# Kernel optimization log

Measured on AMD Instinct MI355X. Metric: run time of the kernel, lower is better.

The kernel has to match this reference:

```python
import jax, jax.numpy as jnp
import numpy as np

N_RET = 8192
N_LGN = 2048
SQUARE_SIZE = 10.0
NEIGHBOURHOOD = 1.0
MU_WTS = 2.5
SIGMA_WTS = 0.14
ETA = 0.1


def setup_inputs() -> dict:
    key = jax.random.key(0)
    ks = jax.random.split(key, 6)
    # retina topology on a [0, square_size]^2 plane
    topo = jax.random.uniform(ks[0], (N_RET, 2), dtype=jnp.float32) * SQUARE_SIZE
    # pairwise distances [N_ret, N_ret]
    d = jnp.sqrt(jnp.sum((topo[:, None, :] - topo[None, :, :]) ** 2, axis=-1))
    # per-node neighbourhood weights: normal(mu, sigma) masked to dist <= neighbourhood_size
    w = MU_WTS + SIGMA_WTS * jax.random.normal(ks[1], (N_RET, N_RET), dtype=jnp.float32)
    retina_weights = jnp.where(d <= NEIGHBOURHOOD, w, 0.0)
    # per-node firing threshold (Node internals: threshold ~ N(70, 2), same family as LGN)
    retina_threshold = 70.0 + 2.0 * jax.random.normal(ks[2], (N_RET,), dtype=jnp.float32)
    # LGN weights, row-normalised to mean mu_wts as in __init__
    lw = MU_WTS + SIGMA_WTS * jax.random.normal(ks[3], (N_LGN, N_RET), dtype=jnp.float32)
    lgn_weights = lw / jnp.mean(lw, axis=1, keepdims=True) * MU_WTS
    lgn_threshold = 70.0 + 2.0 * jax.random.normal(ks[4], (N_LGN,), dtype=jnp.float32)
    is_firing = (jax.random.uniform(ks[5], (N_RET,)) < 0.2).astype(jnp.float32)
    return {
        "retina_weights": retina_weights,
        "retina_threshold": retina_threshold,
        "lgn_weights": lgn_weights,
        "lgn_threshold": lgn_threshold,
        "is_firing": is_firing,
    }


def reference(retina_weights, retina_threshold, lgn_weights, lgn_threshold, is_firing):
    # Per-node sparse neighbourhood matvec (the Python loop over nodes, vectorised):
    node_x = retina_weights @ is_firing                       # [N_ret]
    new_firing = (node_x > retina_threshold).astype(retina_weights.dtype)
    # LGN activation + relu (lgn_act[lgn_act < 0] = 0)
    lgn_act = jnp.maximum(lgn_weights @ new_firing, 0.0)      # [N_lgn]
    act = jnp.maximum(lgn_act - lgn_threshold, 0.0)
    # winner-take-all update of the argmax LGN row
    idx = jnp.argmax(act)
    val = act[idx]
    row = lgn_weights[idx]
    # original does two additions of 0.5 * eta * val * active_neurons
    row = row + 0.5 * (ETA * val * new_firing)
    row = row + 0.5 * (ETA * val * new_firing)
    thr_new = lgn_threshold[idx] + 0.005 * val
    row = row / jnp.mean(row) * MU_WTS
    cond = val > 0
    lgn_weights_new = jnp.where(cond, lgn_weights.at[idx].set(row), lgn_weights)
    lgn_threshold_new = jnp.where(cond, lgn_threshold.at[idx].set(thr_new), lgn_threshold)
    return new_firing, lgn_act, lgn_weights_new, lgn_threshold_new
```

## Files before the change

### kernel.cpp

```cpp
#include <hip/hip_runtime.h>


constexpr int N_RET = 8192;
constexpr int N_LGN = 2048;
constexpr float ETA = 0.1f;
constexpr float MU_WTS = 2.5f;

__global__ __launch_bounds__(256) void k_retina(
    const float* __restrict__ rw, const float* __restrict__ rthr,
    const float* __restrict__ firing, float* __restrict__ new_firing)
{
    const int row = blockIdx.x;
    const int t = threadIdx.x;
    const float4* __restrict__ wr = reinterpret_cast<const float4*>(rw + (size_t)row * N_RET);
    const float4* __restrict__ fr = reinterpret_cast<const float4*>(firing);
    float4 acc = make_float4(0.f, 0.f, 0.f, 0.f);
#pragma unroll
    for (int k = 0; k < (N_RET / 4) / 256; ++k) {
        const int j = t + k * 256;
        const float4 w = wr[j];
        const float4 f = fr[j];
        acc.x += w.x * f.x; acc.y += w.y * f.y;
        acc.z += w.z * f.z; acc.w += w.w * f.w;
    }
    float v = (acc.x + acc.y) + (acc.z + acc.w);
#pragma unroll
    for (int off = 32; off > 0; off >>= 1) v += __shfl_down(v, off, 64);
    __shared__ float s[4];
    const int lane = t & 63, wv = t >> 6;
    if (lane == 0) s[wv] = v;
    __syncthreads();
    if (t == 0) {
        const float x = (s[0] + s[1]) + (s[2] + s[3]);
        new_firing[row] = (x > rthr[row]) ? 1.0f : 0.0f;
    }
}

__global__ __launch_bounds__(256) void k_lgn(
    const float* __restrict__ lw, const float* __restrict__ firing,
    float* __restrict__ lgn_act, float* __restrict__ w_out)
{
    const int row = blockIdx.x;
    const int t = threadIdx.x;
    const float4* __restrict__ wr = reinterpret_cast<const float4*>(lw + (size_t)row * N_RET);
    const float4* __restrict__ fr = reinterpret_cast<const float4*>(firing);
    float4* __restrict__ wo = reinterpret_cast<float4*>(w_out + (size_t)row * N_RET);
    float4 acc = make_float4(0.f, 0.f, 0.f, 0.f);
#pragma unroll
    for (int k = 0; k < (N_RET / 4) / 256; ++k) {
        const int j = t + k * 256;
        const float4 w = wr[j];
        const float4 f = fr[j];
        wo[j] = w;
        acc.x += w.x * f.x; acc.y += w.y * f.y;
        acc.z += w.z * f.z; acc.w += w.w * f.w;
    }
    float v = (acc.x + acc.y) + (acc.z + acc.w);
#pragma unroll
    for (int off = 32; off > 0; off >>= 1) v += __shfl_down(v, off, 64);
    __shared__ float s[4];
    const int lane = t & 63, wv = t >> 6;
    if (lane == 0) s[wv] = v;
    __syncthreads();
    if (t == 0) {
        const float x = (s[0] + s[1]) + (s[2] + s[3]);
        lgn_act[row] = fmaxf(x, 0.0f);
    }
}

__global__ __launch_bounds__(256) void k_argmax(
    const float* __restrict__ lgn_act, const float* __restrict__ lthr,
    float* __restrict__ thr_out, float* __restrict__ ws)
{
    const int t = threadIdx.x;
    float bv = -1.0f;
    int bi = 0x40000000;
    for (int k = 0; k < N_LGN / 256; ++k) {
        const int j = t + k * 256;
        const float a = fmaxf(lgn_act[j] - lthr[j], 0.0f);
        if (a > bv) { bv = a; bi = j; }
    }
#pragma unroll
    for (int off = 32; off > 0; off >>= 1) {
        const float ov = __shfl_down(bv, off, 64);
        const int oi = __shfl_down(bi, off, 64);
        if (ov > bv || (ov == bv && oi < bi)) { bv = ov; bi = oi; }
    }
    __shared__ float sv[4];
    __shared__ int si[4];
    __shared__ float fval;
    __shared__ int fidx;
    const int lane = t & 63, wv = t >> 6;
    if (lane == 0) { sv[wv] = bv; si[wv] = bi; }
    __syncthreads();
    if (t == 0) {
        float v = sv[0]; int i = si[0];
#pragma unroll
        for (int k = 1; k < 4; ++k)
            if (sv[k] > v || (sv[k] == v && si[k] < i)) { v = sv[k]; i = si[k]; }
        fval = v; fidx = i;
        ws[0] = v;
        reinterpret_cast<int*>(ws)[1] = i;
    }
    __syncthreads();
    const float val = fval;
    const int idx = fidx;
    for (int k = 0; k < N_LGN / 256; ++k) {
        const int j = t + k * 256;
        float tv = lthr[j];
        if (val > 0.0f && j == idx) tv += 0.005f * val;
        thr_out[j] = tv;
    }
}

__global__ __launch_bounds__(256) void k_rowupd(
    const float* __restrict__ lw, const float* __restrict__ firing,
    const float* __restrict__ ws, float* __restrict__ w_out)
{
    const float val = ws[0];
    if (!(val > 0.0f)) return;
    const int idx = reinterpret_cast<const int*>(ws)[1];
    const int t = threadIdx.x;
    const float* __restrict__ wr = lw + (size_t)idx * N_RET;
    float* __restrict__ wo = w_out + (size_t)idx * N_RET;
    __shared__ float buf[N_RET];
    const float av = 0.5f * (ETA * val);
    float part = 0.0f;
    for (int k = 0; k < N_RET / 256; ++k) {
        const int j = t + k * 256;
        const float a = (firing[j] != 0.0f) ? av : 0.0f;
        const float x = (wr[j] + a) + a;
        buf[j] = x;
        part += x;
    }
#pragma unroll
    for (int off = 32; off > 0; off >>= 1) part += __shfl_down(part, off, 64);
    __shared__ float s[4];
    __shared__ float mean_s;
    const int lane = t & 63, wv = t >> 6;
    if (lane == 0) s[wv] = part;
    __syncthreads();
    if (t == 0) {
        const float sum = (s[0] + s[1]) + (s[2] + s[3]);
        mean_s = sum / (float)N_RET;
    }
    __syncthreads();
    const float m = mean_s;
    for (int k = 0; k < N_RET / 256; ++k) {
        const int j = t + k * 256;
        wo[j] = buf[j] / m * MU_WTS;
    }
}

extern "C" void kernel_launch(void* const* d_in, const int* in_sizes, int n_in,
                              void* d_out, int out_size, void* d_ws, size_t ws_size,
                              hipStream_t stream)
{
    const float* rw   = (const float*)d_in[0];
    const float* rthr = (const float*)d_in[1];
    const float* lw   = (const float*)d_in[2];
    const float* lthr = (const float*)d_in[3];
    const float* fir  = (const float*)d_in[4];

    float* out   = (float*)d_out;
    float* o_fir = out;
    float* o_act = out + N_RET;
    float* o_w   = out + N_RET + N_LGN;
    float* o_thr = out + N_RET + N_LGN + (size_t)N_LGN * N_RET;
    float* ws    = (float*)d_ws;

    hipLaunchKernelGGL(k_retina, dim3(N_RET), dim3(256), 0, stream, rw, rthr, fir, o_fir);
    hipLaunchKernelGGL(k_lgn,    dim3(N_LGN), dim3(256), 0, stream, lw, o_fir, o_act, o_w);
    hipLaunchKernelGGL(k_argmax, dim3(1),     dim3(256), 0, stream, o_act, lthr, o_thr, ws);
    hipLaunchKernelGGL(k_rowupd, dim3(1),     dim3(256), 0, stream, lw, o_fir, ws, o_w);
}
```

Before: 85.40 us.

## Fuse argmax and row update into one kernel, use nontemporal loads/stores

Merges the argmax and winning-row update kernels into a single 1024-thread block, so one launch and the workspace round-trip are gone and the row stays in registers rather than shared memory. The streaming weight reads in the retina and LGN matvecs, and the copy to the output, now use nontemporal loads and stores to lower cache pollution. The fused tail is still a single block running serially after the LGN pass.

```diff
diff --git a/kernel.cpp b/kernel.cpp
--- a/kernel.cpp
+++ b/kernel.cpp
@@ -6,22 +6,35 @@
 constexpr float ETA = 0.1f;
 constexpr float MU_WTS = 2.5f;
 
+typedef float vf4 __attribute__((ext_vector_type(4)));
+
+__device__ __forceinline__ vf4 ntload4(const float* p) {
+    return __builtin_nontemporal_load(reinterpret_cast<const vf4*>(p));
+}
+__device__ __forceinline__ void ntstore4(float* p, vf4 v) {
+    __builtin_nontemporal_store(v, reinterpret_cast<vf4*>(p));
+}
+__device__ __forceinline__ vf4 ld4(const float* p) {
+    return *reinterpret_cast<const vf4*>(p);
+}
+__device__ __forceinline__ void st4(float* p, vf4 v) {
+    *reinterpret_cast<vf4*>(p) = v;
+}
+
 __global__ __launch_bounds__(256) void k_retina(
     const float* __restrict__ rw, const float* __restrict__ rthr,
     const float* __restrict__ firing, float* __restrict__ new_firing)
 {
     const int row = blockIdx.x;
     const int t = threadIdx.x;
-    const float4* __restrict__ wr = reinterpret_cast<const float4*>(rw + (size_t)row * N_RET);
-    const float4* __restrict__ fr = reinterpret_cast<const float4*>(firing);
-    float4 acc = make_float4(0.f, 0.f, 0.f, 0.f);
+    const float* __restrict__ wr = rw + (size_t)row * N_RET;
+    vf4 acc = (vf4)(0.0f);
 #pragma unroll
     for (int k = 0; k < (N_RET / 4) / 256; ++k) {
-        const int j = t + k * 256;
-        const float4 w = wr[j];
-        const float4 f = fr[j];
-        acc.x += w.x * f.x; acc.y += w.y * f.y;
-        acc.z += w.z * f.z; acc.w += w.w * f.w;
+        const int j = (t + k * 256) * 4;
+        const vf4 w = ntload4(wr + j);
+        const vf4 f = ld4(firing + j);
+        acc += w * f;
     }
     float v = (acc.x + acc.y) + (acc.z + acc.w);
 #pragma unroll
@@ -42,18 +55,16 @@
 {
     const int row = blockIdx.x;
     const int t = threadIdx.x;
-    const float4* __restrict__ wr = reinterpret_cast<const float4*>(lw + (size_t)row * N_RET);
-    const float4* __restrict__ fr = reinterpret_cast<const float4*>(firing);
-    float4* __restrict__ wo = reinterpret_cast<float4*>(w_out + (size_t)row * N_RET);
-    float4 acc = make_float4(0.f, 0.f, 0.f, 0.f);
+    const float* __restrict__ wr = lw + (size_t)row * N_RET;
+    float* __restrict__ wo = w_out + (size_t)row * N_RET;
+    vf4 acc = (vf4)(0.0f);
 #pragma unroll
     for (int k = 0; k < (N_RET / 4) / 256; ++k) {
-        const int j = t + k * 256;
-        const float4 w = wr[j];
-        const float4 f = fr[j];
-        wo[j] = w;
-        acc.x += w.x * f.x; acc.y += w.y * f.y;
-        acc.z += w.z * f.z; acc.w += w.w * f.w;
+        const int j = (t + k * 256) * 4;
+        const vf4 w = ntload4(wr + j);
+        const vf4 f = ld4(firing + j);
+        ntstore4(wo + j, w);
+        acc += w * f;
     }
     float v = (acc.x + acc.y) + (acc.z + acc.w);
 #pragma unroll
@@ -68,15 +79,23 @@
     }
 }
 
-__global__ __launch_bounds__(256) void k_argmax(
+__global__ __launch_bounds__(1024) void k_wta(
     const float* __restrict__ lgn_act, const float* __restrict__ lthr,
-    float* __restrict__ thr_out, float* __restrict__ ws)
+    const float* __restrict__ lw, const float* __restrict__ firing,
+    float* __restrict__ thr_out, float* __restrict__ w_out)
 {
     const int t = threadIdx.x;
+    const int lane = t & 63, wv = t >> 6;
+    __shared__ float sv[16];
+    __shared__ int si[16];
+    __shared__ float s_val;
+    __shared__ int s_idx;
+
     float bv = -1.0f;
     int bi = 0x40000000;
-    for (int k = 0; k < N_LGN / 256; ++k) {
-        const int j = t + k * 256;
+#pragma unroll
+    for (int k = 0; k < N_LGN / 1024; ++k) {
+        const int j = t + k * 1024;
         const float a = fmaxf(lgn_act[j] - lthr[j], 0.0f);
         if (a > bv) { bv = a; bi = j; }
     }
@@ -86,69 +105,61 @@
         const int oi = __shfl_down(bi, off, 64);
         if (ov > bv || (ov == bv && oi < bi)) { bv = ov; bi = oi; }
     }
-    __shared__ float sv[4];
-    __shared__ int si[4];
-    __shared__ float fval;
-    __shared__ int fidx;
-    const int lane = t & 63, wv = t >> 6;
     if (lane == 0) { sv[wv] = bv; si[wv] = bi; }
     __syncthreads();
     if (t == 0) {
         float v = sv[0]; int i = si[0];
 #pragma unroll
-        for (int k = 1; k < 4; ++k)
+        for (int k = 1; k < 16; ++k)
             if (sv[k] > v || (sv[k] == v && si[k] < i)) { v = sv[k]; i = si[k]; }
-        fval = v; fidx = i;
-        ws[0] = v;
-        reinterpret_cast<int*>(ws)[1] = i;
+        s_val = v; s_idx = i;
     }
     __syncthreads();
-    const float val = fval;
-    const int idx = fidx;
-    for (int k = 0; k < N_LGN / 256; ++k) {
-        const int j = t + k * 256;
+    const float val = s_val;
+    const int idx = s_idx;
+
+#pragma unroll
+    for (int k = 0; k < N_LGN / 1024; ++k) {
+        const int j = t + k * 1024;
         float tv = lthr[j];
         if (val > 0.0f && j == idx) tv += 0.005f * val;
         thr_out[j] = tv;
     }
-}
+    if (!(val > 0.0f)) return;
 
-__global__ __launch_bounds__(256) void k_rowupd(
-    const float* __restrict__ lw, const float* __restrict__ firing,
-    const float* __restrict__ ws, float* __restrict__ w_out)
-{
-    const float val = ws[0];
-    if (!(val > 0.0f)) return;
-    const int idx = reinterpret_cast<const int*>(ws)[1];
-    const int t = threadIdx.x;
     const float* __restrict__ wr = lw + (size_t)idx * N_RET;
     float* __restrict__ wo = w_out + (size_t)idx * N_RET;
-    __shared__ float buf[N_RET];
     const float av = 0.5f * (ETA * val);
+
+    vf4 x[2];
     float part = 0.0f;
-    for (int k = 0; k < N_RET / 256; ++k) {
-        const int j = t + k * 256;
-        const float a = (firing[j] != 0.0f) ? av : 0.0f;
-        const float x = (wr[j] + a) + a;
-        buf[j] = x;
-        part += x;
+#pragma unroll
+    for (int k = 0; k < (N_RET / 4) / 1024; ++k) {
+        const int j = (t + k * 1024) * 4;
+        const vf4 w = ld4(wr + j);
+        const vf4 f = ld4(firing + j);
+        vf4 v = (w + av * f) + av * f;
+        x[k] = v;
+        part += (v.x + v.y) + (v.z + v.w);
     }
 #pragma unroll
     for (int off = 32; off > 0; off >>= 1) part += __shfl_down(part, off, 64);
-    __shared__ float s[4];
-    __shared__ float mean_s;
-    const int lane = t & 63, wv = t >> 6;
-    if (lane == 0) s[wv] = part;
+    __shared__ float red[16];
+    __shared__ float s_mean;
+    if (lane == 0) red[wv] = part;
     __syncthreads();
     if (t == 0) {
-        const float sum = (s[0] + s[1]) + (s[2] + s[3]);
-        mean_s = sum / (float)N_RET;
+        float sum = 0.0f;
+#pragma unroll
+        for (int k = 0; k < 16; ++k) sum += red[k];
+        s_mean = sum / (float)N_RET;
     }
     __syncthreads();
-    const float m = mean_s;
-    for (int k = 0; k < N_RET / 256; ++k) {
-        const int j = t + k * 256;
-        wo[j] = buf[j] / m * MU_WTS;
+    const float m = s_mean;
+#pragma unroll
+    for (int k = 0; k < (N_RET / 4) / 1024; ++k) {
+        const int j = (t + k * 1024) * 4;
+        st4(wo + j, x[k] / m * MU_WTS);
     }
 }
 
@@ -167,10 +178,8 @@
     float* o_act = out + N_RET;
     float* o_w   = out + N_RET + N_LGN;
     float* o_thr = out + N_RET + N_LGN + (size_t)N_LGN * N_RET;
-    float* ws    = (float*)d_ws;
 
-    hipLaunchKernelGGL(k_retina, dim3(N_RET), dim3(256), 0, stream, rw, rthr, fir, o_fir);
-    hipLaunchKernelGGL(k_lgn,    dim3(N_LGN), dim3(256), 0, stream, lw, o_fir, o_act, o_w);
-    hipLaunchKernelGGL(k_argmax, dim3(1),     dim3(256), 0, stream, o_act, lthr, o_thr, ws);
-    hipLaunchKernelGGL(k_rowupd, dim3(1),     dim3(256), 0, stream, lw, o_fir, ws, o_w);
+    hipLaunchKernelGGL(k_retina, dim3(N_RET), dim3(256),  0, stream, rw, rthr, fir, o_fir);
+    hipLaunchKernelGGL(k_lgn,    dim3(N_LGN), dim3(256),  0, stream, lw, o_fir, o_act, o_w);
+    hipLaunchKernelGGL(k_wta,    dim3(1),     dim3(1024), 0, stream, o_act, lthr, lw, o_fir, o_thr, o_w);
 }
```

New measurement: 75.83 us. 1.13x faster.
